# Performance work log

Hardware: AMD Instinct MI355X
Metric: run time of the kernel (lower is better)

## Reference

```python
import jax, jax.numpy as jnp
import numpy as np

B, N, D_IN, H, L, HEADS = 8, 1024, 64, 128, 2, 4
HEAD_DIM = H // HEADS
EPS = 1e-5


def setup_inputs() -> dict:
    key = jax.random.key(0)
    ks = jax.random.split(key, 20)
    x = jax.random.normal(ks[0], (B, N, D_IN), dtype=jnp.float32)
    adj = jax.random.randint(ks[1], (B, N, N), 0, 2).astype(jnp.float32)
    s = lambda fan_in: 1.0 / np.sqrt(fan_in)
    enc_w = jax.random.uniform(ks[2], (H, D_IN), minval=-s(D_IN), maxval=s(D_IN))
    enc_b = jax.random.uniform(ks[3], (H,), minval=-s(D_IN), maxval=s(D_IN))
    # per-layer stacked projection weights, torch Linear layout [out,in]
    def mk(k, shape):
        return jax.random.uniform(k, shape, minval=-s(H), maxval=s(H))
    q_w = mk(ks[4], (L, H, H)); q_b = mk(ks[5], (L, H))
    k_w = mk(ks[6], (L, H, H)); k_b = mk(ks[7], (L, H))
    v_w = mk(ks[8], (L, H, H)); v_b = mk(ks[9], (L, H))
    o_w = mk(ks[10], (L, H, H)); o_b = mk(ks[11], (L, H))
    ln_g = jnp.ones((L, H), jnp.float32)
    ln_b = jnp.zeros((L, H), jnp.float32)
    out_w = mk(ks[12], (H, H)); out_b = mk(ks[13], (H,))
    return {"x": x, "adj": adj, "enc_w": enc_w, "enc_b": enc_b,
            "q_w": q_w, "q_b": q_b, "k_w": k_w, "k_b": k_b,
            "v_w": v_w, "v_b": v_b, "o_w": o_w, "o_b": o_b,
            "ln_g": ln_g, "ln_b": ln_b, "out_w": out_w, "out_b": out_b}


def _layernorm(x, g, b):
    mu = jnp.mean(x, axis=-1, keepdims=True)
    var = jnp.var(x, axis=-1, keepdims=True)
    return (x - mu) * jax.lax.rsqrt(var + EPS) * g + b


def _gat_layer(h, adj, qw, qb, kw, kb, vw, vb, ow, ob):
    b, n, _ = h.shape
    q = (h @ qw.T + qb).reshape(b, n, HEADS, HEAD_DIM)
    k = (h @ kw.T + kb).reshape(b, n, HEADS, HEAD_DIM)
    v = (h @ vw.T + vb).reshape(b, n, HEADS, HEAD_DIM)
    scale = HEAD_DIM ** -0.5
    attn = jnp.einsum('bihd,bjhd->bhij', q, k) * scale
    mask = adj[:, None, :, :]  # (b,1,n,n)
    attn = jnp.where(mask == 0, -jnp.inf, attn)
    a = jax.nn.softmax(attn, axis=-1)
    a = jnp.nan_to_num(a, nan=0.0)  # rows with no neighbours -> 0
    out = jnp.einsum('bhij,bjhd->bihd', a, v).reshape(b, n, H)
    return out @ ow.T + ob


def reference(x, adj, enc_w, enc_b, q_w, q_b, k_w, k_b, v_w, v_b,
              o_w, o_b, ln_g, ln_b, out_w, out_b):
    h = jax.nn.relu(x @ enc_w.T + enc_b)
    for i in range(L):
        h_new = _gat_layer(h, adj, q_w[i], q_b[i], k_w[i], k_b[i],
                           v_w[i], v_b[i], o_w[i], o_b[i])
        h = jax.nn.relu(_layernorm(h_new, ln_g[i], ln_b[i])) + h
    return h @ out_w.T + out_b
```

## Files before the change

kernel.cpp:

```cpp
#include <hip/hip_runtime.h>

#define B 8
#define N 1024
#define D_IN 64
#define H 128
#define HEADS 4
#define HD 32
#define L 2
#define EPS 1e-5f
#define NEG_BIG -1e30f
#define SCALE 0.17677669529663687f

typedef __attribute__((ext_vector_type(8))) short bf16x8;
typedef __attribute__((ext_vector_type(4))) float f32x4;

__device__ __forceinline__ unsigned short f2bf(float f) {
    unsigned u = __float_as_uint(f);
    u = u + 0x7fffu + ((u >> 16) & 1u);
    return (unsigned short)(u >> 16);
}
__device__ __forceinline__ float bf2f(unsigned short s) {
    return __uint_as_float(((unsigned)s) << 16);
}
__device__ __forceinline__ void gload_lds16(const void* g, void* l) {
    __builtin_amdgcn_global_load_lds(
        (const __attribute__((address_space(1))) unsigned int*)g,
        (__attribute__((address_space(3))) unsigned int*)l,
        16, 0, 0);
}

__global__ __launch_bounds__(256) void pack_kernel(
    const float* __restrict__ adj, unsigned* __restrict__ mb) {
    int wd = blockIdx.x * 256 + threadIdx.x;
    const float4* src = (const float4*)(adj + (size_t)wd * 32);
    unsigned m = 0;
    #pragma unroll
    for (int c = 0; c < 8; ++c) {
        float4 f = src[c];
        if (f.x != 0.0f) m |= 1u << (c * 4 + 0);
        if (f.y != 0.0f) m |= 1u << (c * 4 + 1);
        if (f.z != 0.0f) m |= 1u << (c * 4 + 2);
        if (f.w != 0.0f) m |= 1u << (c * 4 + 3);
    }
    mb[wd] = m;
}

__global__ __launch_bounds__(256) void prep_kernel(
    const float* __restrict__ x, const float* __restrict__ enc_w,
    const float* __restrict__ q_w, const float* __restrict__ k_w,
    const float* __restrict__ v_w, const float* __restrict__ q_b,
    const float* __restrict__ k_b, const float* __restrict__ v_b,
    const float* __restrict__ o_w, const float* __restrict__ out_w,
    unsigned short* __restrict__ x_bf, unsigned short* __restrict__ wenc,
    unsigned short* __restrict__ wqkv, float* __restrict__ bqkv,
    unsigned short* __restrict__ woh, unsigned short* __restrict__ wol,
    unsigned short* __restrict__ wfh, unsigned short* __restrict__ wfl) {
    int id = blockIdx.x * 256 + threadIdx.x;
    const int XN = B * N * D_IN;
    const int WE = H * D_IN;
    const int WQ = L * 3 * H * H;
    const int BQ = L * 3 * H;
    const int WO = L * H * H;
    const int WF = H * H;
    if (id < XN) { x_bf[id] = f2bf(x[id]); return; }
    id -= XN;
    if (id < WE) { wenc[id] = f2bf(enc_w[id]); return; }
    id -= WE;
    if (id < WQ) {
        int layer = id / (3 * H * H);
        int r = id % (3 * H * H);
        int mat = r / (H * H);
        int e = r % (H * H);
        const float* src = mat == 0 ? q_w : (mat == 1 ? k_w : v_w);
        float f = src[layer * H * H + e];
        if (mat == 0) f *= SCALE;
        wqkv[id] = f2bf(f);
        return;
    }
    id -= WQ;
    if (id < BQ) {
        int layer = id / (3 * H);
        int r = id % (3 * H);
        int mat = r / H;
        int e = r % H;
        const float* src = mat == 0 ? q_b : (mat == 1 ? k_b : v_b);
        float f = src[layer * H + e];
        if (mat == 0) f *= SCALE;
        bqkv[id] = f;
        return;
    }
    id -= BQ;
    if (id < WO) {
        float f = o_w[id];
        unsigned short hi = f2bf(f);
        woh[id] = hi;
        wol[id] = f2bf(f - bf2f(hi));
        return;
    }
    id -= WO;
    if (id < WF) {
        float f = out_w[id];
        unsigned short hi = f2bf(f);
        wfh[id] = hi;
        wfl[id] = f2bf(f - bf2f(hi));
    }
}

__global__ __launch_bounds__(256) void enc_kernel(
    const unsigned short* __restrict__ x_bf, const unsigned short* __restrict__ wenc,
    const float* __restrict__ eb, float* __restrict__ h, unsigned short* __restrict__ h_bf) {
    __shared__ unsigned short wt[H * D_IN];
    __shared__ unsigned short at[64 * D_IN];
    const int t = threadIdx.x;
    const int r0 = blockIdx.x * 64;
    const int w = t >> 6, lane = t & 63, g = lane >> 4, c16 = lane & 15;

    #pragma unroll
    for (int i = 0; i < 4; ++i) {
        int ci = i * 256 + t, row = ci >> 3, cr = ci & 7;
        gload_lds16(wenc + row * 64 + (cr ^ (row & 7)) * 8, (char*)wt + (i * 4 + w) * 1024);
    }
    #pragma unroll
    for (int i = 0; i < 2; ++i) {
        int ci = i * 256 + t, row = ci >> 3, cr = ci & 7;
        gload_lds16(x_bf + (size_t)(r0 + row) * 64 + (cr ^ (row & 7)) * 8,
                    (char*)at + (i * 4 + w) * 1024);
    }
    __syncthreads();

    const int arow = w * 16 + c16;
    bf16x8 a0 = *(const bf16x8*)(at + arow * 64 + ((g ^ (arow & 7)) * 8));
    bf16x8 a1 = *(const bf16x8*)(at + arow * 64 + (((4 + g) ^ (arow & 7)) * 8));
    f32x4 acc[8];
    #pragma unroll
    for (int sub = 0; sub < 8; ++sub) {
        int bcol = sub * 16 + c16;
        bf16x8 b0 = *(const bf16x8*)(wt + bcol * 64 + ((g ^ (bcol & 7)) * 8));
        bf16x8 b1 = *(const bf16x8*)(wt + bcol * 64 + (((4 + g) ^ (bcol & 7)) * 8));
        f32x4 z = {0.f, 0.f, 0.f, 0.f};
        z = __builtin_amdgcn_mfma_f32_16x16x32_bf16(a0, b0, z, 0, 0, 0);
        acc[sub] = __builtin_amdgcn_mfma_f32_16x16x32_bf16(a1, b1, z, 0, 0, 0);
    }
    #pragma unroll
    for (int sub = 0; sub < 8; ++sub) {
        int col = sub * 16 + c16;
        float bias = eb[col];
        #pragma unroll
        for (int rr = 0; rr < 4; ++rr) {
            int row = r0 + w * 16 + g * 4 + rr;
            float v = fmaxf(acc[sub][rr] + bias, 0.0f);
            h[(size_t)row * H + col] = v;
            h_bf[(size_t)row * H + col] = f2bf(v);
        }
    }
}

__global__ __launch_bounds__(256) void qkv_kernel(
    const unsigned short* __restrict__ h_bf, const unsigned short* __restrict__ wqkv_l,
    const float* __restrict__ bqkv_l,
    unsigned short* __restrict__ q, unsigned short* __restrict__ k,
    unsigned short* __restrict__ vT) {
    __shared__ unsigned short wt[384 * 128];
    __shared__ unsigned short at[64 * 128];
    const int t = threadIdx.x;
    const int r0 = blockIdx.x * 64;
    const int w = t >> 6, lane = t & 63, g = lane >> 4, c16 = lane & 15;

    #pragma unroll
    for (int i = 0; i < 24; ++i) {
        int ci = i * 256 + t, row = ci >> 4, cr = ci & 15;
        gload_lds16(wqkv_l + (size_t)row * 128 + (cr ^ (row & 7)) * 8,
                    (char*)wt + (i * 4 + w) * 1024);
    }
    #pragma unroll
    for (int i = 0; i < 4; ++i) {
        int ci = i * 256 + t, row = ci >> 4, cr = ci & 15;
        gload_lds16(h_bf + (size_t)(r0 + row) * 128 + (cr ^ (row & 7)) * 8,
                    (char*)at + (i * 4 + w) * 1024);
    }
    __syncthreads();

    const int arow = w * 16 + c16;
    bf16x8 a[4];
    #pragma unroll
    for (int ks = 0; ks < 4; ++ks)
        a[ks] = *(const bf16x8*)(at + arow * 128 + (((ks * 4 + g) ^ (arow & 7)) * 8));

    f32x4 acc[24];
    #pragma unroll
    for (int sub = 0; sub < 24; ++sub) {
        int bcol = sub * 16 + c16;
        f32x4 z = {0.f, 0.f, 0.f, 0.f};
        #pragma unroll
        for (int ks = 0; ks < 4; ++ks) {
            bf16x8 bb = *(const bf16x8*)(wt + (size_t)bcol * 128 + (((ks * 4 + g) ^ (bcol & 7)) * 8));
            z = __builtin_amdgcn_mfma_f32_16x16x32_bf16(a[ks], bb, z, 0, 0, 0);
        }
        acc[sub] = z;
    }
    #pragma unroll
    for (int sub = 0; sub < 24; ++sub) {
        int mat = sub >> 3;
        int col = (sub & 7) * 16 + c16;
        float bias = bqkv_l[mat * H + col];
        if (mat < 2) {
            unsigned short* dst = mat == 0 ? q : k;
            #pragma unroll
            for (int rr = 0; rr < 4; ++rr) {
                int row = r0 + w * 16 + g * 4 + rr;
                dst[(size_t)row * H + col] = f2bf(acc[sub][rr] + bias);
            }
        } else {
            int hd = col >> 5, d = col & 31;
            int bb = r0 >> 10;
            int jbase = (r0 & (N - 1)) + w * 16 + g * 4;
            int pos = (jbase & ~63) + ((((jbase >> 3) & 7) ^ (d & 7)) << 3) + (jbase & 7);
            float v0 = acc[sub][0] + bias, v1 = acc[sub][1] + bias;
            float v2 = acc[sub][2] + bias, v3 = acc[sub][3] + bias;
            unsigned lo, hi;
            asm("v_cvt_pk_bf16_f32 %0, %1, %2" : "=v"(lo) : "v"(v0), "v"(v1));
            asm("v_cvt_pk_bf16_f32 %0, %1, %2" : "=v"(hi) : "v"(v2), "v"(v3));
            uint2 pk2; pk2.x = lo; pk2.y = hi;
            *(uint2*)(vT + ((size_t)(bb * HEADS + hd) * HD + d) * N + pos) = pk2;
        }
    }
}

__global__ __launch_bounds__(256) void attn_kernel(
    const unsigned short* __restrict__ qg, const unsigned short* __restrict__ kg,
    const unsigned short* __restrict__ vTg, const unsigned* __restrict__ mb,
    float* __restrict__ ao) {
    __shared__ unsigned short qt[64 * 32];
    __shared__ unsigned short kt[2][64 * 32];
    __shared__ unsigned short vt[2][32 * 64];
    __shared__ unsigned short pl[4][16 * 72];

    const int bid = blockIdx.x;
    const int itile = bid & 15;
    const int head = (bid >> 4) & 3;
    const int b = bid >> 6;
    const int i0 = itile * 64;
    const int bh = b * HEADS + head;

    const int t = threadIdx.x;
    const int w = t >> 6;
    const int lane = t & 63;
    const int g = lane >> 4;
    const int c16 = lane & 15;

    const int srow = t >> 2;
    const int sch = (t & 3) ^ ((t >> 2) & 3);

    gload_lds16(qg + ((size_t)(b * N + i0 + srow)) * H + head * HD + sch * 8,
                (char*)qt + w * 1024);
    gload_lds16(kg + ((size_t)(b * N + srow)) * H + head * HD + sch * 8,
                (char*)kt[0] + w * 1024);
    gload_lds16(vTg + ((size_t)bh * HD + (t >> 3)) * N + (t & 7) * 8,
                (char*)vt[0] + w * 1024);

    const unsigned* mrow = mb + (size_t)(b * N + i0 + w * 16 + c16) * (N / 32);
    unsigned long long am = *(const unsigned long long*)mrow;

    __syncthreads();

    const int swq = c16 & 3;
    const bf16x8 qfrag = *(const bf16x8*)(qt + (w * 16 + c16) * 32 + ((g ^ swq) * 8));

    f32x4 oacc[2];
    oacc[0] = (f32x4){0.f, 0.f, 0.f, 0.f};
    oacc[1] = (f32x4){0.f, 0.f, 0.f, 0.f};
    float mrun = NEG_BIG, lrun = 0.0f;

    for (int jt = 0; jt < 16; ++jt) {
        const int cur = jt & 1;
        unsigned long long amn;
        if (jt < 15) {
            const int j0n = (jt + 1) * 64;
            gload_lds16(kg + ((size_t)(b * N + j0n + srow)) * H + head * HD + sch * 8,
                        (char*)kt[cur ^ 1] + w * 1024);
            gload_lds16(vTg + ((size_t)bh * HD + (t >> 3)) * N + j0n + (t & 7) * 8,
                        (char*)vt[cur ^ 1] + w * 1024);
            amn = *(const unsigned long long*)(mrow + (jt + 1) * 2);
        }
        f32x4 sacc[4];
        #pragma unroll
        for (int jsub = 0; jsub < 4; ++jsub) {
            bf16x8 kfrag = *(const bf16x8*)(kt[cur] + (jsub * 16 + c16) * 32 + ((g ^ swq) * 8));
            f32x4 z = {0.f, 0.f, 0.f, 0.f};
            sacc[jsub] = __builtin_amdgcn_mfma_f32_16x16x32_bf16(kfrag, qfrag, z, 0, 0, 0);
        }
        unsigned long long amg = am >> (g * 4);
        float sm[4][4], p[4][4];
        float mx = NEG_BIG;
        #pragma unroll
        for (int jsub = 0; jsub < 4; ++jsub)
            #pragma unroll
            for (int r = 0; r < 4; ++r) {
                bool alive = (amg >> (jsub * 16 + r)) & 1ull;
                float s = alive ? sacc[jsub][r] : NEG_BIG;
                sm[jsub][r] = s;
                mx = fmaxf(mx, s);
            }
        mx = fmaxf(mx, __shfl_xor(mx, 16));
        mx = fmaxf(mx, __shfl_xor(mx, 32));
        float mnew = fmaxf(mrun, mx);
        float sf = __expf(mrun - mnew);
        mrun = mnew;
        float rs = 0.0f;
        #pragma unroll
        for (int jsub = 0; jsub < 4; ++jsub)
            #pragma unroll
            for (int r = 0; r < 4; ++r) {
                float pv = (sm[jsub][r] > -0.9e30f) ? __expf(sm[jsub][r] - mnew) : 0.0f;
                p[jsub][r] = pv;
                rs += pv;
            }
        rs += __shfl_xor(rs, 16);
        rs += __shfl_xor(rs, 32);
        lrun = lrun * sf + rs;
        #pragma unroll
        for (int jsub = 0; jsub < 4; ++jsub) {
            unsigned lo, hi;
            asm("v_cvt_pk_bf16_f32 %0, %1, %2" : "=v"(lo) : "v"(p[jsub][0]), "v"(p[jsub][1]));
            asm("v_cvt_pk_bf16_f32 %0, %1, %2" : "=v"(hi) : "v"(p[jsub][2]), "v"(p[jsub][3]));
            uint2 pk2; pk2.x = lo; pk2.y = hi;
            *(uint2*)(&pl[w][c16 * 72 + jsub * 16 + g * 4]) = pk2;
        }
        #pragma unroll
        for (int dsub = 0; dsub < 2; ++dsub)
            #pragma unroll
            for (int r = 0; r < 4; ++r)
                oacc[dsub][r] *= sf;
        asm volatile("s_waitcnt lgkmcnt(0)" ::: "memory");
        #pragma unroll
        for (int ks = 0; ks < 2; ++ks) {
            bf16x8 pa = *(const bf16x8*)(&pl[w][c16 * 72 + ks * 32 + g * 8]);
            #pragma unroll
            for (int dsub = 0; dsub < 2; ++dsub) {
                bf16x8 va = *(const bf16x8*)(vt[cur] + (dsub * 16 + c16) * 64 +
                                             (((ks * 4 + g) ^ (c16 & 7)) * 8));
                oacc[dsub] = __builtin_amdgcn_mfma_f32_16x16x32_bf16(va, pa, oacc[dsub], 0, 0, 0);
            }
        }
        if (jt < 15) {
            am = amn;
            __syncthreads();
        }
    }
    float inv = (lrun > 0.0f) ? (1.0f / lrun) : 0.0f;
    #pragma unroll
    for (int dsub = 0; dsub < 2; ++dsub) {
        float4 o;
        o.x = oacc[dsub][0] * inv; o.y = oacc[dsub][1] * inv;
        o.z = oacc[dsub][2] * inv; o.w = oacc[dsub][3] * inv;
        *(float4*)(ao + ((size_t)(b * N + i0 + w * 16 + c16)) * H +
                   head * HD + dsub * 16 + g * 4) = o;
    }
}

__device__ __forceinline__ void stage_split(
    const float* __restrict__ src, unsigned short* hi, unsigned short* lo, int t) {
    #pragma unroll
    for (int it = 0; it < 8; ++it) {
        int idx4 = it * 256 + t;
        int row = idx4 >> 5, c4 = (idx4 & 31) * 4;
        float4 f = ((const float4*)src)[idx4];
        unsigned short h0 = f2bf(f.x), h1 = f2bf(f.y), h2 = f2bf(f.z), h3 = f2bf(f.w);
        unsigned short l0 = f2bf(f.x - bf2f(h0)), l1 = f2bf(f.y - bf2f(h1));
        unsigned short l2 = f2bf(f.z - bf2f(h2)), l3 = f2bf(f.w - bf2f(h3));
        *(unsigned*)(hi + row * 130 + c4)     = (unsigned)h0 | ((unsigned)h1 << 16);
        *(unsigned*)(hi + row * 130 + c4 + 2) = (unsigned)h2 | ((unsigned)h3 << 16);
        *(unsigned*)(lo + row * 130 + c4)     = (unsigned)l0 | ((unsigned)l1 << 16);
        *(unsigned*)(lo + row * 130 + c4 + 2) = (unsigned)l2 | ((unsigned)l3 << 16);
    }
}

__device__ __forceinline__ void split_gemm(
    const unsigned short* ah, const unsigned short* al,
    const unsigned short* wh, const unsigned short* wl,
    int arow, int g, int c16, f32x4* acc) {
    bf16x8 ahf[4], alf[4];
    #pragma unroll
    for (int ks = 0; ks < 4; ++ks) {
        ahf[ks] = *(const bf16x8*)(ah + arow * 130 + ks * 32 + g * 8);
        alf[ks] = *(const bf16x8*)(al + arow * 130 + ks * 32 + g * 8);
    }
    #pragma unroll
    for (int sub = 0; sub < 8; ++sub) {
        int bcol = sub * 16 + c16;
        f32x4 z = {0.f, 0.f, 0.f, 0.f};
        #pragma unroll
        for (int ks = 0; ks < 4; ++ks) {
            bf16x8 bh = *(const bf16x8*)(wh + bcol * 128 + (((ks * 4 + g) ^ (bcol & 7)) * 8));
            bf16x8 bl = *(const bf16x8*)(wl + bcol * 128 + (((ks * 4 + g) ^ (bcol & 7)) * 8));
            z = __builtin_amdgcn_mfma_f32_16x16x32_bf16(ahf[ks], bh, z, 0, 0, 0);
            z = __builtin_amdgcn_mfma_f32_16x16x32_bf16(alf[ks], bh, z, 0, 0, 0);
            z = __builtin_amdgcn_mfma_f32_16x16x32_bf16(ahf[ks], bl, z, 0, 0, 0);
        }
        acc[sub] = z;
    }
}

__device__ __forceinline__ void stage_w(const unsigned short* __restrict__ src,
                                        unsigned short* dst, int t, int w) {
    #pragma unroll
    for (int i = 0; i < 8; ++i) {
        int ci = i * 256 + t, row = ci >> 4, cr = ci & 15;
        gload_lds16(src + (size_t)row * 128 + (cr ^ (row & 7)) * 8,
                    (char*)dst + (i * 4 + w) * 1024);
    }
}

__global__ __launch_bounds__(256) void oln_kernel(
    const float* __restrict__ ao, const unsigned short* __restrict__ woh_l,
    const unsigned short* __restrict__ wol_l, const float* __restrict__ ob,
    const float* __restrict__ lng, const float* __restrict__ lnb,
    float* __restrict__ h, unsigned short* __restrict__ h_bf) {
    __shared__ unsigned short ah[64 * 130], al[64 * 130];
    __shared__ unsigned short wh[128 * 128], wl[128 * 128];
    const int t = threadIdx.x;
    const int r0 = blockIdx.x * 64;
    const int w = t >> 6, lane = t & 63, g = lane >> 4, c16 = lane & 15;

    stage_w(woh_l, wh, t, w);
    stage_w(wol_l, wl, t, w);
    stage_split(ao + (size_t)r0 * H, ah, al, t);
    __syncthreads();

    const int arow = w * 16 + c16;
    f32x4 acc[8];
    split_gemm(ah, al, wh, wl, arow, g, c16, acc);

    float val[8][4], s1[4] = {0, 0, 0, 0}, s2[4] = {0, 0, 0, 0};
    #pragma unroll
    for (int sub = 0; sub < 8; ++sub) {
        int col = sub * 16 + c16;
        float bias = ob[col];
        #pragma unroll
        for (int rr = 0; rr < 4; ++rr) {
            float vv = acc[sub][rr] + bias;
            val[sub][rr] = vv;
            s1[rr] += vv;
            s2[rr] += vv * vv;
        }
    }
    #pragma unroll
    for (int rr = 0; rr < 4; ++rr) {
        #pragma unroll
        for (int off = 1; off < 16; off <<= 1) {
            s1[rr] += __shfl_xor(s1[rr], off);
            s2[rr] += __shfl_xor(s2[rr], off);
        }
    }
    #pragma unroll
    for (int rr = 0; rr < 4; ++rr) {
        float mu = s1[rr] * (1.0f / H);
        float var = s2[rr] * (1.0f / H) - mu * mu;
        float rsn = rsqrtf(var + EPS);
        int row = r0 + w * 16 + g * 4 + rr;
        #pragma unroll
        for (int sub = 0; sub < 8; ++sub) {
            int col = sub * 16 + c16;
            float y = (val[sub][rr] - mu) * rsn * lng[col] + lnb[col];
            float hn = fmaxf(y, 0.0f) + h[(size_t)row * H + col];
            h[(size_t)row * H + col] = hn;
            h_bf[(size_t)row * H + col] = f2bf(hn);
        }
    }
}

__global__ __launch_bounds__(256) void olnfinal_kernel(
    const float* __restrict__ ao, const unsigned short* __restrict__ woh_l,
    const unsigned short* __restrict__ wol_l, const float* __restrict__ ob,
    const float* __restrict__ lng, const float* __restrict__ lnb,
    const float* __restrict__ h, const unsigned short* __restrict__ wfh,
    const unsigned short* __restrict__ wfl, const float* __restrict__ fb,
    float* __restrict__ out) {
    __shared__ unsigned short ah[64 * 130], al[64 * 130];
    __shared__ unsigned short wh[128 * 128], wl[128 * 128];
    const int t = threadIdx.x;
    const int r0 = blockIdx.x * 64;
    const int w = t >> 6, lane = t & 63, g = lane >> 4, c16 = lane & 15;

    stage_w(woh_l, wh, t, w);
    stage_w(wol_l, wl, t, w);
    stage_split(ao + (size_t)r0 * H, ah, al, t);
    __syncthreads();

    const int arow = w * 16 + c16;
    f32x4 acc[8];
    split_gemm(ah, al, wh, wl, arow, g, c16, acc);

    float val[8][4], s1[4] = {0, 0, 0, 0}, s2[4] = {0, 0, 0, 0};
    #pragma unroll
    for (int sub = 0; sub < 8; ++sub) {
        int col = sub * 16 + c16;
        float bias = ob[col];
        #pragma unroll
        for (int rr = 0; rr < 4; ++rr) {
            float vv = acc[sub][rr] + bias;
            val[sub][rr] = vv;
            s1[rr] += vv;
            s2[rr] += vv * vv;
        }
    }
    #pragma unroll
    for (int rr = 0; rr < 4; ++rr) {
        #pragma unroll
        for (int off = 1; off < 16; off <<= 1) {
            s1[rr] += __shfl_xor(s1[rr], off);
            s2[rr] += __shfl_xor(s2[rr], off);
        }
    }
    __syncthreads();
    #pragma unroll
    for (int rr = 0; rr < 4; ++rr) {
        float mu = s1[rr] * (1.0f / H);
        float var = s2[rr] * (1.0f / H) - mu * mu;
        float rsn = rsqrtf(var + EPS);
        int row = w * 16 + g * 4 + rr;
        #pragma unroll
        for (int sub = 0; sub < 8; ++sub) {
            int col = sub * 16 + c16;
            float y = (val[sub][rr] - mu) * rsn * lng[col] + lnb[col];
            float hn = fmaxf(y, 0.0f) + h[(size_t)(r0 + row) * H + col];
            unsigned short hi = f2bf(hn);
            ah[row * 130 + col] = hi;
            al[row * 130 + col] = f2bf(hn - bf2f(hi));
        }
    }
    stage_w(wfh, wh, t, w);
    stage_w(wfl, wl, t, w);
    __syncthreads();

    f32x4 fac[8];
    split_gemm(ah, al, wh, wl, arow, g, c16, fac);
    #pragma unroll
    for (int sub = 0; sub < 8; ++sub) {
        int col = sub * 16 + c16;
        float bias = fb[col];
        #pragma unroll
        for (int rr = 0; rr < 4; ++rr) {
            int row = r0 + w * 16 + g * 4 + rr;
            out[(size_t)row * H + col] = fac[sub][rr] + bias;
        }
    }
}

extern "C" void kernel_launch(void* const* d_in, const int* in_sizes, int n_in,
                              void* d_out, int out_size, void* d_ws, size_t ws_size,
                              hipStream_t stream) {
    const float* x     = (const float*)d_in[0];
    const float* adj   = (const float*)d_in[1];
    const float* enc_w = (const float*)d_in[2];
    const float* enc_b = (const float*)d_in[3];
    const float* q_w   = (const float*)d_in[4];
    const float* q_b   = (const float*)d_in[5];
    const float* k_w   = (const float*)d_in[6];
    const float* k_b   = (const float*)d_in[7];
    const float* v_w   = (const float*)d_in[8];
    const float* v_b   = (const float*)d_in[9];
    const float* o_w   = (const float*)d_in[10];
    const float* o_b   = (const float*)d_in[11];
    const float* ln_g  = (const float*)d_in[12];
    const float* ln_b  = (const float*)d_in[13];
    const float* out_w = (const float*)d_in[14];
    const float* out_b = (const float*)d_in[15];

    const size_t BNH = (size_t)B * N * H;
    float* h  = (float*)d_ws;
    float* ao = h + BNH;
    unsigned short* h_bf = (unsigned short*)(ao + BNH);
    unsigned short* qb = h_bf + BNH;
    unsigned short* kb = qb + BNH;
    unsigned short* vT = kb + BNH;
    unsigned* mbits = (unsigned*)(vT + BNH);
    unsigned short* x_bf = (unsigned short*)(mbits + (size_t)B * N * N / 32);
    unsigned short* wenc = x_bf + (size_t)B * N * D_IN;
    unsigned short* wqkv = wenc + H * D_IN;
    float* bqkv = (float*)(wqkv + (size_t)L * 3 * H * H);
    unsigned short* woh = (unsigned short*)(bqkv + L * 3 * H);
    unsigned short* wol = woh + (size_t)L * H * H;
    unsigned short* wfh = wol + (size_t)L * H * H;
    unsigned short* wfl = wfh + (size_t)H * H;

    pack_kernel<<<B * N * N / 32 / 256, 256, 0, stream>>>(adj, mbits);
    const int prep_total = B * N * D_IN + H * D_IN + L * 3 * H * H + L * 3 * H
                         + L * H * H + H * H;
    prep_kernel<<<(prep_total + 255) / 256, 256, 0, stream>>>(
        x, enc_w, q_w, k_w, v_w, q_b, k_b, v_b, o_w, out_w,
        x_bf, wenc, wqkv, bqkv, woh, wol, wfh, wfl);
    enc_kernel<<<B * N / 64, 256, 0, stream>>>(x_bf, wenc, enc_b, h, h_bf);

    qkv_kernel<<<B * N / 64, 256, 0, stream>>>(h_bf, wqkv, bqkv, qb, kb, vT);
    attn_kernel<<<B * HEADS * (N / 64), 256, 0, stream>>>(qb, kb, vT, mbits, ao);
    oln_kernel<<<B * N / 64, 256, 0, stream>>>(
        ao, woh, wol, o_b, ln_g, ln_b, h, h_bf);
    qkv_kernel<<<B * N / 64, 256, 0, stream>>>(
        h_bf, wqkv + (size_t)3 * H * H, bqkv + 3 * H, qb, kb, vT);
    attn_kernel<<<B * HEADS * (N / 64), 256, 0, stream>>>(qb, kb, vT, mbits, ao);
    olnfinal_kernel<<<B * N / 64, 256, 0, stream>>>(
        ao, woh + (size_t)H * H, wol + (size_t)H * H, o_b + H,
        ln_g + H, ln_b + H, h, wfh, wfl, out_b, (float*)d_out);
}
```

Measured before the change: 100.1 us.

## Split QKV projection across two blocks per row tile and widen attention key tile

The QKV kernel now launches two blocks per 64-row tile, each loading and computing half of the 384 output columns. This halves per-block LDS (96KB to 48KB) and accumulator registers to raise occupancy, at the cost of loading the activation tile twice. The attention kernel processes 128 keys per iteration instead of 64, halving loop trips and barriers. In exchange it uses more LDS and registers per block, which could lower occupancy.

Result: faster. 95.21 us (-4.9%).

```diff
diff --git a/kernel.cpp b/kernel.cpp
--- a/kernel.cpp
+++ b/kernel.cpp
@@ -160,16 +160,18 @@
     const float* __restrict__ bqkv_l,
     unsigned short* __restrict__ q, unsigned short* __restrict__ k,
     unsigned short* __restrict__ vT) {
-    __shared__ unsigned short wt[384 * 128];
+    __shared__ unsigned short wt[192 * 128];
     __shared__ unsigned short at[64 * 128];
     const int t = threadIdx.x;
-    const int r0 = blockIdx.x * 64;
+    const int r0 = (blockIdx.x >> 1) * 64;
+    const int ch = blockIdx.x & 1;
     const int w = t >> 6, lane = t & 63, g = lane >> 4, c16 = lane & 15;
-
-    #pragma unroll
-    for (int i = 0; i < 24; ++i) {
+    const unsigned short* wsrc = wqkv_l + (size_t)ch * 192 * 128;
+
+    #pragma unroll
+    for (int i = 0; i < 12; ++i) {
         int ci = i * 256 + t, row = ci >> 4, cr = ci & 15;
-        gload_lds16(wqkv_l + (size_t)row * 128 + (cr ^ (row & 7)) * 8,
+        gload_lds16(wsrc + (size_t)row * 128 + (cr ^ (row & 7)) * 8,
                     (char*)wt + (i * 4 + w) * 1024);
     }
     #pragma unroll
@@ -186,9 +188,9 @@
     for (int ks = 0; ks < 4; ++ks)
         a[ks] = *(const bf16x8*)(at + arow * 128 + (((ks * 4 + g) ^ (arow & 7)) * 8));
 
-    f32x4 acc[24];
-    #pragma unroll
-    for (int sub = 0; sub < 24; ++sub) {
+    f32x4 acc[12];
+    #pragma unroll
+    for (int sub = 0; sub < 12; ++sub) {
         int bcol = sub * 16 + c16;
         f32x4 z = {0.f, 0.f, 0.f, 0.f};
         #pragma unroll
@@ -199,19 +201,20 @@
         acc[sub] = z;
     }
     #pragma unroll
-    for (int sub = 0; sub < 24; ++sub) {
-        int mat = sub >> 3;
-        int col = (sub & 7) * 16 + c16;
-        float bias = bqkv_l[mat * H + col];
+    for (int sub = 0; sub < 12; ++sub) {
+        int gcol = ch * 192 + sub * 16 + c16;
+        int mat = gcol >> 7;
+        int colin = gcol & 127;
+        float bias = bqkv_l[mat * H + colin];
         if (mat < 2) {
             unsigned short* dst = mat == 0 ? q : k;
             #pragma unroll
             for (int rr = 0; rr < 4; ++rr) {
                 int row = r0 + w * 16 + g * 4 + rr;
-                dst[(size_t)row * H + col] = f2bf(acc[sub][rr] + bias);
+                dst[(size_t)row * H + colin] = f2bf(acc[sub][rr] + bias);
             }
         } else {
-            int hd = col >> 5, d = col & 31;
+            int hd = colin >> 5, d = colin & 31;
             int bb = r0 >> 10;
             int jbase = (r0 & (N - 1)) + w * 16 + g * 4;
             int pos = (jbase & ~63) + ((((jbase >> 3) & 7) ^ (d & 7)) << 3) + (jbase & 7);
@@ -231,9 +234,9 @@
     const unsigned short* __restrict__ vTg, const unsigned* __restrict__ mb,
     float* __restrict__ ao) {
     __shared__ unsigned short qt[64 * 32];
-    __shared__ unsigned short kt[2][64 * 32];
-    __shared__ unsigned short vt[2][32 * 64];
-    __shared__ unsigned short pl[4][16 * 72];
+    __shared__ unsigned short kt[2][128 * 32];
+    __shared__ unsigned short vt[2][32 * 128];
+    __shared__ unsigned short pl[4][16 * 136];
 
     const int bid = blockIdx.x;
     const int itile = bid & 15;
@@ -253,13 +256,18 @@
 
     gload_lds16(qg + ((size_t)(b * N + i0 + srow)) * H + head * HD + sch * 8,
                 (char*)qt + w * 1024);
-    gload_lds16(kg + ((size_t)(b * N + srow)) * H + head * HD + sch * 8,
-                (char*)kt[0] + w * 1024);
-    gload_lds16(vTg + ((size_t)bh * HD + (t >> 3)) * N + (t & 7) * 8,
-                (char*)vt[0] + w * 1024);
-
+    #pragma unroll
+    for (int i = 0; i < 2; ++i)
+        gload_lds16(kg + ((size_t)(b * N + i * 64 + srow)) * H + head * HD + sch * 8,
+                    (char*)kt[0] + i * 4096 + w * 1024);
+    #pragma unroll
+    for (int i = 0; i < 2; ++i) {
+        int d = i * 16 + (t >> 4), c = t & 15;
+        gload_lds16(vTg + ((size_t)bh * HD + d) * N + c * 8,
+                    (char*)vt[0] + i * 4096 + w * 1024);
+    }
     const unsigned* mrow = mb + (size_t)(b * N + i0 + w * 16 + c16) * (N / 32);
-    unsigned long long am = *(const unsigned long long*)mrow;
+    uint4 am = *(const uint4*)mrow;
 
     __syncthreads();
 
@@ -271,36 +279,43 @@
     oacc[1] = (f32x4){0.f, 0.f, 0.f, 0.f};
     float mrun = NEG_BIG, lrun = 0.0f;
 
-    for (int jt = 0; jt < 16; ++jt) {
+    for (int jt = 0; jt < 8; ++jt) {
         const int cur = jt & 1;
-        unsigned long long amn;
-        if (jt < 15) {
-            const int j0n = (jt + 1) * 64;
-            gload_lds16(kg + ((size_t)(b * N + j0n + srow)) * H + head * HD + sch * 8,
-                        (char*)kt[cur ^ 1] + w * 1024);
-            gload_lds16(vTg + ((size_t)bh * HD + (t >> 3)) * N + j0n + (t & 7) * 8,
-                        (char*)vt[cur ^ 1] + w * 1024);
-            amn = *(const unsigned long long*)(mrow + (jt + 1) * 2);
-        }
-        f32x4 sacc[4];
-        #pragma unroll
-        for (int jsub = 0; jsub < 4; ++jsub) {
+        uint4 amn;
+        if (jt < 7) {
+            const int j0n = (jt + 1) * 128;
+            #pragma unroll
+            for (int i = 0; i < 2; ++i)
+                gload_lds16(kg + ((size_t)(b * N + j0n + i * 64 + srow)) * H + head * HD + sch * 8,
+                            (char*)kt[cur ^ 1] + i * 4096 + w * 1024);
+            #pragma unroll
+            for (int i = 0; i < 2; ++i) {
+                int d = i * 16 + (t >> 4), c = t & 15;
+                gload_lds16(vTg + ((size_t)bh * HD + d) * N + j0n + c * 8,
+                            (char*)vt[cur ^ 1] + i * 4096 + w * 1024);
+            }
+            amn = *(const uint4*)(mrow + (jt + 1) * 4);
+        }
+        f32x4 sacc[8];
+        #pragma unroll
+        for (int jsub = 0; jsub < 8; ++jsub) {
             bf16x8 kfrag = *(const bf16x8*)(kt[cur] + (jsub * 16 + c16) * 32 + ((g ^ swq) * 8));
             f32x4 z = {0.f, 0.f, 0.f, 0.f};
             sacc[jsub] = __builtin_amdgcn_mfma_f32_16x16x32_bf16(kfrag, qfrag, z, 0, 0, 0);
         }
-        unsigned long long amg = am >> (g * 4);
-        float sm[4][4], p[4][4];
         float mx = NEG_BIG;
         #pragma unroll
-        for (int jsub = 0; jsub < 4; ++jsub)
+        for (int jsub = 0; jsub < 8; ++jsub) {
+            int wsel = jsub >> 1;
+            unsigned mw = wsel == 0 ? am.x : wsel == 1 ? am.y : wsel == 2 ? am.z : am.w;
             #pragma unroll
             for (int r = 0; r < 4; ++r) {
-                bool alive = (amg >> (jsub * 16 + r)) & 1ull;
+                bool alive = (mw >> ((jsub & 1) * 16 + g * 4 + r)) & 1u;
                 float s = alive ? sacc[jsub][r] : NEG_BIG;
-                sm[jsub][r] = s;
+                sacc[jsub][r] = s;
                 mx = fmaxf(mx, s);
             }
+        }
         mx = fmaxf(mx, __shfl_xor(mx, 16));
         mx = fmaxf(mx, __shfl_xor(mx, 32));
         float mnew = fmaxf(mrun, mx);
@@ -308,23 +323,23 @@
         mrun = mnew;
         float rs = 0.0f;
         #pragma unroll
-        for (int jsub = 0; jsub < 4; ++jsub)
+        for (int jsub = 0; jsub < 8; ++jsub)
             #pragma unroll
             for (int r = 0; r < 4; ++r) {
-                float pv = (sm[jsub][r] > -0.9e30f) ? __expf(sm[jsub][r] - mnew) : 0.0f;
-                p[jsub][r] = pv;
+                float pv = (sacc[jsub][r] > -0.9e30f) ? __expf(sacc[jsub][r] - mnew) : 0.0f;
+                sacc[jsub][r] = pv;
                 rs += pv;
             }
         rs += __shfl_xor(rs, 16);
         rs += __shfl_xor(rs, 32);
         lrun = lrun * sf + rs;
         #pragma unroll
-        for (int jsub = 0; jsub < 4; ++jsub) {
+        for (int jsub = 0; jsub < 8; ++jsub) {
             unsigned lo, hi;
-            asm("v_cvt_pk_bf16_f32 %0, %1, %2" : "=v"(lo) : "v"(p[jsub][0]), "v"(p[jsub][1]));
-            asm("v_cvt_pk_bf16_f32 %0, %1, %2" : "=v"(hi) : "v"(p[jsub][2]), "v"(p[jsub][3]));
+            asm("v_cvt_pk_bf16_f32 %0, %1, %2" : "=v"(lo) : "v"(sacc[jsub][0]), "v"(sacc[jsub][1]));
+            asm("v_cvt_pk_bf16_f32 %0, %1, %2" : "=v"(hi) : "v"(sacc[jsub][2]), "v"(sacc[jsub][3]));
             uint2 pk2; pk2.x = lo; pk2.y = hi;
-            *(uint2*)(&pl[w][c16 * 72 + jsub * 16 + g * 4]) = pk2;
+            *(uint2*)(&pl[w][c16 * 136 + jsub * 16 + g * 4]) = pk2;
         }
         #pragma unroll
         for (int dsub = 0; dsub < 2; ++dsub)
@@ -333,16 +348,17 @@
                 oacc[dsub][r] *= sf;
         asm volatile("s_waitcnt lgkmcnt(0)" ::: "memory");
         #pragma unroll
-        for (int ks = 0; ks < 2; ++ks) {
-            bf16x8 pa = *(const bf16x8*)(&pl[w][c16 * 72 + ks * 32 + g * 8]);
+        for (int ks = 0; ks < 4; ++ks) {
+            bf16x8 pa = *(const bf16x8*)(&pl[w][c16 * 136 + ks * 32 + g * 8]);
             #pragma unroll
             for (int dsub = 0; dsub < 2; ++dsub) {
-                bf16x8 va = *(const bf16x8*)(vt[cur] + (dsub * 16 + c16) * 64 +
-                                             (((ks * 4 + g) ^ (c16 & 7)) * 8));
+                int cj = ks * 4 + g;
+                bf16x8 va = *(const bf16x8*)(vt[cur] + (dsub * 16 + c16) * 128 +
+                                             (cj >> 3) * 64 + (((cj & 7) ^ (c16 & 7)) * 8));
                 oacc[dsub] = __builtin_amdgcn_mfma_f32_16x16x32_bf16(va, pa, oacc[dsub], 0, 0, 0);
             }
         }
-        if (jt < 15) {
+        if (jt < 7) {
             am = amn;
             __syncthreads();
         }
@@ -592,11 +608,11 @@
         x_bf, wenc, wqkv, bqkv, woh, wol, wfh, wfl);
     enc_kernel<<<B * N / 64, 256, 0, stream>>>(x_bf, wenc, enc_b, h, h_bf);
 
-    qkv_kernel<<<B * N / 64, 256, 0, stream>>>(h_bf, wqkv, bqkv, qb, kb, vT);
+    qkv_kernel<<<B * N / 32, 256, 0, stream>>>(h_bf, wqkv, bqkv, qb, kb, vT);
     attn_kernel<<<B * HEADS * (N / 64), 256, 0, stream>>>(qb, kb, vT, mbits, ao);
     oln_kernel<<<B * N / 64, 256, 0, stream>>>(
         ao, woh, wol, o_b, ln_g, ln_b, h, h_bf);
-    qkv_kernel<<<B * N / 64, 256, 0, stream>>>(
+    qkv_kernel<<<B * N / 32, 256, 0, stream>>>(
         h_bf, wqkv + (size_t)3 * H * H, bqkv + 3 * H, qb, kb, vT);
     attn_kernel<<<B * HEADS * (N / 64), 256, 0, stream>>>(qb, kb, vT, mbits, ao);
     olnfinal_kernel<<<B * N / 64, 256, 0, stream>>>(
```
